# Performance work log

Hardware: AMD Instinct MI355X
Metric: run time of the kernel (lower is better)

The kernel has to match this reference:

```python
import jax, jax.numpy as jnp
import numpy as np

B, V, W, H = 512, 256, 64, 64  # batch, num_variables, window, hidden_size


def setup_inputs() -> dict:
    key = jax.random.key(0)
    ks = jax.random.split(key, 10)
    s = 0.05
    return {
        "x": jax.random.normal(ks[0], (B, V, W), dtype=jnp.float32),
        # nn.LSTM(input=V, hidden=H): gate order i, f, g, o
        "w_ih": jax.random.normal(ks[1], (4 * H, V), dtype=jnp.float32) * s,
        "w_hh": jax.random.normal(ks[2], (4 * H, H), dtype=jnp.float32) * s,
        "b_ih": jax.random.normal(ks[3], (4 * H,), dtype=jnp.float32) * s,
        "b_hh": jax.random.normal(ks[4], (4 * H,), dtype=jnp.float32) * s,
        # linear_v: Linear(window, 1, bias=False)
        "w_v": jax.random.normal(ks[5], (1, W), dtype=jnp.float32) * s,
        # linear_w: Linear(2H, window)
        "w_w": jax.random.normal(ks[6], (W, 2 * H), dtype=jnp.float32) * s,
        "b_w": jax.random.normal(ks[7], (W,), dtype=jnp.float32) * s,
        # linear_u: Linear(window, window)
        "w_u": jax.random.normal(ks[8], (W, W), dtype=jnp.float32) * s,
        "b_u": jax.random.normal(ks[9], (W,), dtype=jnp.float32) * s,
    }


def reference(x, w_ih, w_hh, b_ih, b_hh, w_v, w_w, b_w, w_u, b_u):
    batch, n_var, window = x.shape
    hidden = w_hh.shape[1]
    # linear_u over the window (last) dim: (B, V, W)
    u_out = jnp.einsum("bvw,uw->bvu", x, w_u) + b_u
    x_steps = jnp.transpose(x, (2, 0, 1))  # (W, B, V)

    def step(carry, x_t):
        h, c = carry  # each (B, H)
        # input attention
        wout = jnp.concatenate([h, c], axis=1) @ w_w.T + b_w          # (B, W)
        score = jnp.einsum("bvw,w->bv", jnp.tanh(wout[:, None, :] + u_out), w_v[0])
        alpha = jax.nn.softmax(score, axis=1)                          # (B, V)
        x_tilde = alpha * x_t                                          # (B, V)
        # LSTM cell (torch gate order i, f, g, o)
        gates = x_tilde @ w_ih.T + b_ih + h @ w_hh.T + b_hh            # (B, 4H)
        i_g, f_g, g_g, o_g = jnp.split(gates, 4, axis=1)
        i_g = jax.nn.sigmoid(i_g)
        f_g = jax.nn.sigmoid(f_g)
        g_g = jnp.tanh(g_g)
        o_g = jax.nn.sigmoid(o_g)
        c_new = f_g * c + i_g * g_g
        h_new = o_g * jnp.tanh(c_new)
        return (h_new, c_new), (x_tilde, h_new)

    init = (jnp.zeros((batch, hidden), x.dtype), jnp.zeros((batch, hidden), x.dtype))
    _, (x_tilde_seq, h_seq) = jax.lax.scan(step, init, x_steps)
    # matches torch.stack(x_tilde_list) (W,B,V) and torch.stack(h_list) (W,B,H)
    return x_tilde_seq, h_seq
```

## Files before the change

### kernel.cpp

```cpp
#include <hip/hip_runtime.h>


#define KLOG2E  1.4426950408889634f
#define K2LOG2E 2.8853900817779268f

typedef _Float16 h2 __attribute__((ext_vector_type(2)));
union H2U { h2 h; unsigned u; };

__device__ __forceinline__ float frcp(float x)  { return __builtin_amdgcn_rcpf(x); }
__device__ __forceinline__ float fexp2(float x) { return __builtin_amdgcn_exp2f(x); }
__device__ __forceinline__ float fsigmoid(float x) { return frcp(1.f + fexp2(-KLOG2E * x)); }
__device__ __forceinline__ float ftanh(float x) { return 1.f - 2.f * frcp(fexp2(K2LOG2E * x) + 1.f); }

#if __has_builtin(__builtin_amdgcn_fdot2)
__device__ __forceinline__ float fdot2(h2 a, h2 b, float c) { return __builtin_amdgcn_fdot2(a, b, c, false); }
#else
__device__ __forceinline__ float fdot2(h2 a, h2 b, float c) { return c + (float)a.x*(float)b.x + (float)a.y*(float)b.y; }
#endif

__device__ __forceinline__ unsigned pkrtz_u(float a, float b) {
#if __has_builtin(__builtin_amdgcn_cvt_pkrtz)
    H2U r; r.h = __builtin_bit_cast(h2, __builtin_amdgcn_cvt_pkrtz(a, b)); return r.u;
#else
    H2U r; r.h.x = (_Float16)a; r.h.y = (_Float16)b; return r.u;
#endif
}
__device__ __forceinline__ h2 pk_rtn(float a, float b) {
    h2 r; r.x = (_Float16)a; r.y = (_Float16)b; return r;
}

#define L_EA   0
#define L_EB   17408
#define L_PSA  34816
#define L_PSB  35328
#define L_EXFA 35840
#define L_EXFB 36096
#define L_XHA  36352
#define L_XHB  36480
#define L_EWA  36608
#define L_EWB  36672
#define L_HCA  36736
#define L_HCB  36864
#define L_HHA  36992
#define L_HHB  37024
#define L_BI   37056
#define L_WV   37312
#define L_WS   37376
#define L_TOT  37392

__global__ __launch_bounds__(512, 2) void enc_kernel(
    const float* __restrict__ x,
    const float* __restrict__ w_ih,
    const float* __restrict__ w_hh,
    const float* __restrict__ b_ih,
    const float* __restrict__ b_hh,
    const float* __restrict__ w_v,
    const float* __restrict__ w_w,
    const float* __restrict__ b_w,
    const float* __restrict__ w_u,
    const float* __restrict__ b_u,
    float* __restrict__ out_xt,
    float* __restrict__ out_h)
{
    extern __shared__ float lds[];
    float*    EA   = lds + L_EA;    float*    EB   = lds + L_EB;
    float*    psA  = lds + L_PSA;   float*    psB  = lds + L_PSB;
    float*    exfA = lds + L_EXFA;  float*    exfB = lds + L_EXFB;
    unsigned* xhA  = (unsigned*)(lds + L_XHA);
    unsigned* xhB  = (unsigned*)(lds + L_XHB);
    float*    ewA  = lds + L_EWA;   float*    ewB  = lds + L_EWB;
    float*    hcA  = lds + L_HCA;   float*    hcB  = lds + L_HCB;
    unsigned* hhA  = (unsigned*)(lds + L_HHA);
    unsigned* hhB  = (unsigned*)(lds + L_HHB);
    float*    biasL= lds + L_BI;
    float*    wv2L = lds + L_WV;
    float*    wsum = lds + L_WS;

    const int tid  = threadIdx.x;
    const int lane = tid & 63;
    const int wvi  = tid >> 6;
    const int bA   = blockIdx.x;
    const int bB   = blockIdx.x + 256;
    const int j    = tid & 255;
    const int sg   = tid >> 8;

    if (tid < 256) biasL[tid] = b_ih[tid] + b_hh[tid];
    if (tid < 64)  wv2L[tid] = -2.f * w_v[tid];
    if (tid < 128) { hcA[tid] = 0.f; hcB[tid] = 0.f; }
    if (tid < 32)  { hhA[tid] = 0u; hhB[tid] = 0u; }

    float Sv = 0.f;
#pragma unroll
    for (int wi = 0; wi < 64; ++wi) Sv += w_v[wi];
    const float bu_lane = b_u[lane];

#pragma unroll 1
    for (int bb = 0; bb < 2; ++bb) {
        float* E = bb ? EB : EA;
        const int b = bb ? bB : bA;
#pragma unroll 1
        for (int half = 0; half < 2; ++half) {
            float4 wu_r[8];
#pragma unroll
            for (int i = 0; i < 8; ++i)
                wu_r[i] = *(const float4*)&w_u[lane*64 + half*32 + 4*i];
            const float* xb = x + b*16384 + half*32;
#pragma unroll 2
            for (int vi = 0; vi < 32; ++vi) {
                int v = __builtin_amdgcn_readfirstlane(wvi*32 + vi);
                const float4* xr = (const float4*)(xb + v*64);
                float acc = 0.f;
#pragma unroll
                for (int i = 0; i < 8; ++i) {
                    float4 xx = xr[i]; float4 wu = wu_r[i];
                    acc += xx.x*wu.x + xx.y*wu.y + xx.z*wu.z + xx.w*wu.w;
                }
                if (half == 0) E[v*68 + lane] = acc + bu_lane;
                else           E[v*68 + lane] = fexp2(K2LOG2E * (E[v*68 + lane] + acc));
            }
        }
    }
    __syncthreads();

    h2 wihr2[64];
    {
        const float4* g4 = (const float4*)(w_ih + j*256 + sg*128);
#pragma unroll
        for (int i = 0; i < 32; ++i) {
            float4 v4 = g4[i];
            wihr2[2*i]     = pk_rtn(v4.x, v4.y);
            wihr2[2*i + 1] = pk_rtn(v4.z, v4.w);
        }
    }
    h2 whh2[16];
    {
        const float4* h4 = (const float4*)(w_hh + j*64 + sg*32);
#pragma unroll
        for (int i = 0; i < 8; ++i) {
            float4 v4 = h4[i];
            whh2[2*i]     = pk_rtn(v4.x, v4.y);
            whh2[2*i + 1] = pk_rtn(v4.z, v4.w);
        }
    }
    const int w8 = wvi*8 + (lane & 7);
    const int kg = lane >> 3;
    float4 www4[4];
#pragma unroll
    for (int m = 0; m < 4; ++m)
        www4[m] = *(const float4*)&w_w[w8*128 + kg*4 + 32*m];
    const float bwr = b_w[w8];

    const float* xrow = x + (sg ? bB : bA)*16384 + j*64;
    const float* Erow = (sg ? EB : EA) + j*68;
    const float* ewX  = sg ? ewB : ewA;
    float*       exfX = sg ? exfB : exfA;
    unsigned*    xhX  = sg ? xhB : xhA;
    float xcur = xrow[0];

    for (int t = 0; t < 64; ++t) {
        {
            float accA = 0.f, accB = 0.f;
#pragma unroll
            for (int m = 0; m < 4; ++m) {
                float4 w4 = www4[m];
                float4 hA = *(const float4*)&hcA[kg*4 + 32*m];
                float4 hB = *(const float4*)&hcB[kg*4 + 32*m];
                accA += hA.x*w4.x + hA.y*w4.y + hA.z*w4.z + hA.w*w4.w;
                accB += hB.x*w4.x + hB.y*w4.y + hB.z*w4.z + hB.w*w4.w;
            }
#pragma unroll
            for (int off = 8; off <= 32; off <<= 1) {
                accA += __shfl_xor(accA, off, 64);
                accB += __shfl_xor(accB, off, 64);
            }
            if (kg == 0)      ewA[w8] = fexp2(K2LOG2E * (accA + bwr));
            else if (kg == 1) ewB[w8] = fexp2(K2LOG2E * (accB + bwr));
        }
        float xnxt = (t < 63) ? xrow[t + 1] : 0.f;
        __syncthreads();

        {
            float acc = Sv;
#pragma unroll
            for (int q = 0; q < 16; ++q) {
                float4 e4 = *(const float4*)&Erow[4*q];
                float4 c4 = *(const float4*)&ewX[4*q];
                float4 v4 = *(const float4*)&wv2L[4*q];
                acc += v4.x * frcp(e4.x*c4.x + 1.f);
                acc += v4.y * frcp(e4.y*c4.y + 1.f);
                acc += v4.z * frcp(e4.z*c4.z + 1.f);
                acc += v4.w * frcp(e4.w*c4.w + 1.f);
            }
            float e  = fexp2(KLOG2E * acc);
            float ex = e * xcur;
            float s = e;
#pragma unroll
            for (int off = 1; off <= 32; off <<= 1) s += __shfl_xor(s, off, 64);
            if (lane == 0) wsum[wvi] = s;
            exfX[j] = ex;
            float exp2v = __shfl_xor(ex, 1, 64);
            if (!(lane & 1)) xhX[j >> 1] = pkrtz_u(ex, exp2v);
        }
        xcur = xnxt;
        __syncthreads();

        {
            float rA = frcp((wsum[0] + wsum[1]) + (wsum[2] + wsum[3]));
            float rB = frcp((wsum[4] + wsum[5]) + (wsum[6] + wsum[7]));
            if (sg == 0) out_xt[t*131072 + bA*256 + j] = rA * exfA[j];
            else         out_xt[t*131072 + bB*256 + j] = rB * exfB[j];

            float aA = 0.f, aB = 0.f;
            const uint4* xxA = (const uint4*)xhA + sg*16;
            const uint4* xxB = (const uint4*)xhB + sg*16;
#pragma unroll
            for (int i = 0; i < 16; ++i) {
                uint4 ua = xxA[i], ub = xxB[i];
                H2U a0, a1, a2, a3, b0, b1, b2, b3;
                a0.u = ua.x; a1.u = ua.y; a2.u = ua.z; a3.u = ua.w;
                b0.u = ub.x; b1.u = ub.y; b2.u = ub.z; b3.u = ub.w;
                aA = fdot2(a0.h, wihr2[4*i + 0], aA);
                aA = fdot2(a1.h, wihr2[4*i + 1], aA);
                aA = fdot2(a2.h, wihr2[4*i + 2], aA);
                aA = fdot2(a3.h, wihr2[4*i + 3], aA);
                aB = fdot2(b0.h, wihr2[4*i + 0], aB);
                aB = fdot2(b1.h, wihr2[4*i + 1], aB);
                aB = fdot2(b2.h, wihr2[4*i + 2], aB);
                aB = fdot2(b3.h, wihr2[4*i + 3], aB);
            }
            float ahA = 0.f, ahB = 0.f;
            const uint4* hha = (const uint4*)hhA + sg*4;
            const uint4* hhb = (const uint4*)hhB + sg*4;
#pragma unroll
            for (int i = 0; i < 4; ++i) {
                uint4 ua = hha[i], ub = hhb[i];
                H2U a0, a1, a2, a3, b0, b1, b2, b3;
                a0.u = ua.x; a1.u = ua.y; a2.u = ua.z; a3.u = ua.w;
                b0.u = ub.x; b1.u = ub.y; b2.u = ub.z; b3.u = ub.w;
                ahA = fdot2(a0.h, whh2[4*i + 0], ahA);
                ahA = fdot2(a1.h, whh2[4*i + 1], ahA);
                ahA = fdot2(a2.h, whh2[4*i + 2], ahA);
                ahA = fdot2(a3.h, whh2[4*i + 3], ahA);
                ahB = fdot2(b0.h, whh2[4*i + 0], ahB);
                ahB = fdot2(b1.h, whh2[4*i + 1], ahB);
                ahB = fdot2(b2.h, whh2[4*i + 2], ahB);
                ahB = fdot2(b3.h, whh2[4*i + 3], ahB);
            }
            psA[sg*256 + j] = rA*aA + ahA;
            psB[sg*256 + j] = rB*aB + ahB;
        }
        __syncthreads();

        if (wvi < 2) {
            float*    ps = wvi ? psB : psA;
            float*    hc = wvi ? hcB : hcA;
            unsigned* hh = wvi ? hhB : hhA;
            float*    oh = out_h + t*32768 + (wvi ? bB : bA)*64;
            const int k = lane;
            float gi = biasL[k      ] + ps[k      ] + ps[256 + k      ];
            float gf = biasL[64  + k] + ps[64  + k] + ps[256 + 64  + k];
            float gg = biasL[128 + k] + ps[128 + k] + ps[256 + 128 + k];
            float go = biasL[192 + k] + ps[192 + k] + ps[256 + 192 + k];
            gi = fsigmoid(gi); gf = fsigmoid(gf);
            gg = ftanh(gg);    go = fsigmoid(go);
            float cn = gf * hc[64 + k] + gi * gg;
            float hn = go * ftanh(cn);
            hc[k] = hn; hc[64 + k] = cn;
            float hp = __shfl_xor(hn, 1, 64);
            if (!(lane & 1)) hh[k >> 1] = pkrtz_u(hn, hp);
            oh[k] = hn;
        }
        __syncthreads();
    }
}

extern "C" void kernel_launch(void* const* d_in, const int* in_sizes, int n_in,
                              void* d_out, int out_size, void* d_ws, size_t ws_size,
                              hipStream_t stream) {
    const float* x    = (const float*)d_in[0];
    const float* w_ih = (const float*)d_in[1];
    const float* w_hh = (const float*)d_in[2];
    const float* b_ih = (const float*)d_in[3];
    const float* b_hh = (const float*)d_in[4];
    const float* w_v  = (const float*)d_in[5];
    const float* w_w  = (const float*)d_in[6];
    const float* b_w  = (const float*)d_in[7];
    const float* w_u  = (const float*)d_in[8];
    const float* b_u  = (const float*)d_in[9];

    float* out_xt = (float*)d_out;
    float* out_h  = out_xt + 64*512*256;

    const size_t shbytes = (size_t)L_TOT * sizeof(float);
    (void)hipFuncSetAttribute((const void*)enc_kernel,
                        hipFuncAttributeMaxDynamicSharedMemorySize, (int)shbytes);
    enc_kernel<<<dim3(256), dim3(512), shbytes, stream>>>(
        x, w_ih, w_hh, b_ih, b_hh, w_v, w_w, b_w, w_u, b_u, out_xt, out_h);
}
```

Before: 337.3 us.

## Double threads per block and split recurrent step work across 1024 threads

Raises the block from 512 to 1024 threads and spreads every phase of the serial recurrence over them. The attention score is split across two half-waves, the w_w projection uses 8-lane groups per output, and the gate dot products are split four ways with a larger partial-sum buffer. The aim is a shorter per-timestep critical path in the latency-bound 64-step loop. In exchange it adds more shuffles and more barrier participants, and the register budget per thread is tighter under launch_bounds(1024,1).

```diff
diff --git a/kernel.cpp b/kernel.cpp
--- a/kernel.cpp
+++ b/kernel.cpp
@@ -32,23 +32,23 @@
 #define L_EA   0
 #define L_EB   17408
 #define L_PSA  34816
-#define L_PSB  35328
-#define L_EXFA 35840
-#define L_EXFB 36096
-#define L_XHA  36352
-#define L_XHB  36480
-#define L_EWA  36608
-#define L_EWB  36672
-#define L_HCA  36736
-#define L_HCB  36864
-#define L_HHA  36992
-#define L_HHB  37024
-#define L_BI   37056
-#define L_WV   37312
-#define L_WS   37376
-#define L_TOT  37392
-
-__global__ __launch_bounds__(512, 2) void enc_kernel(
+#define L_PSB  35840
+#define L_EXFA 36864
+#define L_EXFB 37120
+#define L_XHA  37376
+#define L_XHB  37504
+#define L_EWA  37632
+#define L_EWB  37696
+#define L_HCA  37760
+#define L_HCB  37888
+#define L_HHA  38016
+#define L_HHB  38048
+#define L_BI   38080
+#define L_WV   38336
+#define L_WS   38400
+#define L_TOT  38416
+
+__global__ __launch_bounds__(1024, 1) void enc_kernel(
     const float* __restrict__ x,
     const float* __restrict__ w_ih,
     const float* __restrict__ w_hh,
@@ -81,8 +81,15 @@
     const int wvi  = tid >> 6;
     const int bA   = blockIdx.x;
     const int bB   = blockIdx.x + 256;
-    const int j    = tid & 255;
-    const int sg   = tid >> 8;
+
+    const int j4  = tid & 255;
+    const int sgq = tid >> 8;
+    const int p1b = tid >> 9;
+    const int w8  = (tid >> 3) & 63;
+    const int kg  = tid & 7;
+    const int p2b   = wvi >> 3;
+    const int v2    = ((wvi & 7) << 5) + (lane & 31);
+    const int half2 = lane >> 5;
 
     if (tid < 256) biasL[tid] = b_ih[tid] + b_hh[tid];
     if (tid < 64)  wv2L[tid] = -2.f * w_v[tid];
@@ -106,8 +113,8 @@
                 wu_r[i] = *(const float4*)&w_u[lane*64 + half*32 + 4*i];
             const float* xb = x + b*16384 + half*32;
 #pragma unroll 2
-            for (int vi = 0; vi < 32; ++vi) {
-                int v = __builtin_amdgcn_readfirstlane(wvi*32 + vi);
+            for (int vi = 0; vi < 16; ++vi) {
+                int v = __builtin_amdgcn_readfirstlane(wvi*16 + vi);
                 const float4* xr = (const float4*)(xb + v*64);
                 float acc = 0.f;
 #pragma unroll
@@ -122,99 +129,105 @@
     }
     __syncthreads();
 
-    h2 wihr2[64];
+    h2 wihr2[32];
     {
-        const float4* g4 = (const float4*)(w_ih + j*256 + sg*128);
-#pragma unroll
-        for (int i = 0; i < 32; ++i) {
+        const float4* g4 = (const float4*)(w_ih + j4*256 + sgq*64);
+#pragma unroll
+        for (int i = 0; i < 16; ++i) {
             float4 v4 = g4[i];
             wihr2[2*i]     = pk_rtn(v4.x, v4.y);
             wihr2[2*i + 1] = pk_rtn(v4.z, v4.w);
         }
     }
-    h2 whh2[16];
+    h2 whh2[8];
     {
-        const float4* h4 = (const float4*)(w_hh + j*64 + sg*32);
-#pragma unroll
-        for (int i = 0; i < 8; ++i) {
+        const float4* h4 = (const float4*)(w_hh + j4*64 + sgq*16);
+#pragma unroll
+        for (int i = 0; i < 4; ++i) {
             float4 v4 = h4[i];
             whh2[2*i]     = pk_rtn(v4.x, v4.y);
             whh2[2*i + 1] = pk_rtn(v4.z, v4.w);
         }
     }
-    const int w8 = wvi*8 + (lane & 7);
-    const int kg = lane >> 3;
-    float4 www4[4];
-#pragma unroll
-    for (int m = 0; m < 4; ++m)
-        www4[m] = *(const float4*)&w_w[w8*128 + kg*4 + 32*m];
+    float4 www0 = *(const float4*)&w_w[w8*128 + kg*8];
+    float4 www1 = *(const float4*)&w_w[w8*128 + kg*8 + 4];
     const float bwr = b_w[w8];
 
-    const float* xrow = x + (sg ? bB : bA)*16384 + j*64;
-    const float* Erow = (sg ? EB : EA) + j*68;
-    const float* ewX  = sg ? ewB : ewA;
-    float*       exfX = sg ? exfB : exfA;
-    unsigned*    xhX  = sg ? xhB : xhA;
-    float xcur = xrow[0];
+    const float* xrow = x + (p2b ? bB : bA)*16384 + v2*64;
+    float xcur = (half2 == 0) ? xrow[0] : 0.f;
 
     for (int t = 0; t < 64; ++t) {
         {
-            float accA = 0.f, accB = 0.f;
-#pragma unroll
-            for (int m = 0; m < 4; ++m) {
-                float4 w4 = www4[m];
-                float4 hA = *(const float4*)&hcA[kg*4 + 32*m];
-                float4 hB = *(const float4*)&hcB[kg*4 + 32*m];
-                accA += hA.x*w4.x + hA.y*w4.y + hA.z*w4.z + hA.w*w4.w;
-                accB += hB.x*w4.x + hB.y*w4.y + hB.z*w4.z + hB.w*w4.w;
-            }
-#pragma unroll
-            for (int off = 8; off <= 32; off <<= 1) {
-                accA += __shfl_xor(accA, off, 64);
-                accB += __shfl_xor(accB, off, 64);
-            }
-            if (kg == 0)      ewA[w8] = fexp2(K2LOG2E * (accA + bwr));
-            else if (kg == 1) ewB[w8] = fexp2(K2LOG2E * (accB + bwr));
-        }
-        float xnxt = (t < 63) ? xrow[t + 1] : 0.f;
+            const float* hcx = p1b ? hcB : hcA;
+            float4 h0 = *(const float4*)&hcx[kg*8];
+            float4 h1 = *(const float4*)&hcx[kg*8 + 4];
+            float acc = h0.x*www0.x + h0.y*www0.y + h0.z*www0.z + h0.w*www0.w
+                      + h1.x*www1.x + h1.y*www1.y + h1.z*www1.z + h1.w*www1.w;
+            acc += __shfl_xor(acc, 1, 64);
+            acc += __shfl_xor(acc, 2, 64);
+            acc += __shfl_xor(acc, 4, 64);
+            if (kg == 0) (p1b ? ewB : ewA)[w8] = fexp2(K2LOG2E * (acc + bwr));
+        }
+        float xnxt = (half2 == 0 && t < 63) ? xrow[t + 1] : 0.f;
         __syncthreads();
 
         {
-            float acc = Sv;
-#pragma unroll
-            for (int q = 0; q < 16; ++q) {
+            const float* Erow = (p2b ? EB : EA) + v2*68 + half2*32;
+            const float* ewX  = (p2b ? ewB : ewA) + half2*32;
+            const float* wvX  = wv2L + half2*32;
+            float a0 = 0.f, a1 = 0.f;
+#pragma unroll
+            for (int q = 0; q < 4; ++q) {
                 float4 e4 = *(const float4*)&Erow[4*q];
                 float4 c4 = *(const float4*)&ewX[4*q];
-                float4 v4 = *(const float4*)&wv2L[4*q];
-                acc += v4.x * frcp(e4.x*c4.x + 1.f);
-                acc += v4.y * frcp(e4.y*c4.y + 1.f);
-                acc += v4.z * frcp(e4.z*c4.z + 1.f);
-                acc += v4.w * frcp(e4.w*c4.w + 1.f);
-            }
+                float4 v4 = *(const float4*)&wvX[4*q];
+                a0 += v4.x * frcp(e4.x*c4.x + 1.f);
+                a0 += v4.y * frcp(e4.y*c4.y + 1.f);
+                a0 += v4.z * frcp(e4.z*c4.z + 1.f);
+                a0 += v4.w * frcp(e4.w*c4.w + 1.f);
+            }
+#pragma unroll
+            for (int q = 4; q < 8; ++q) {
+                float4 e4 = *(const float4*)&Erow[4*q];
+                float4 c4 = *(const float4*)&ewX[4*q];
+                float4 v4 = *(const float4*)&wvX[4*q];
+                a1 += v4.x * frcp(e4.x*c4.x + 1.f);
+                a1 += v4.y * frcp(e4.y*c4.y + 1.f);
+                a1 += v4.z * frcp(e4.z*c4.z + 1.f);
+                a1 += v4.w * frcp(e4.w*c4.w + 1.f);
+            }
+            float acc = a0 + a1 + (half2 ? 0.f : Sv);
+            acc += __shfl_xor(acc, 32, 64);
             float e  = fexp2(KLOG2E * acc);
             float ex = e * xcur;
             float s = e;
-#pragma unroll
-            for (int off = 1; off <= 32; off <<= 1) s += __shfl_xor(s, off, 64);
+            s += __shfl_xor(s, 1, 64);  s += __shfl_xor(s, 2, 64);
+            s += __shfl_xor(s, 4, 64);  s += __shfl_xor(s, 8, 64);
+            s += __shfl_xor(s, 16, 64);
             if (lane == 0) wsum[wvi] = s;
-            exfX[j] = ex;
-            float exp2v = __shfl_xor(ex, 1, 64);
-            if (!(lane & 1)) xhX[j >> 1] = pkrtz_u(ex, exp2v);
+            if (half2 == 0) {
+                (p2b ? exfB : exfA)[v2] = ex;
+                float ex2 = __shfl_xor(ex, 1, 64);
+                if (!(lane & 1)) (p2b ? xhB : xhA)[v2 >> 1] = pkrtz_u(ex, ex2);
+            }
         }
         xcur = xnxt;
         __syncthreads();
 
         {
-            float rA = frcp((wsum[0] + wsum[1]) + (wsum[2] + wsum[3]));
-            float rB = frcp((wsum[4] + wsum[5]) + (wsum[6] + wsum[7]));
-            if (sg == 0) out_xt[t*131072 + bA*256 + j] = rA * exfA[j];
-            else         out_xt[t*131072 + bB*256 + j] = rB * exfB[j];
+            float rA = ((wsum[0] + wsum[1]) + (wsum[2] + wsum[3]))
+                     + ((wsum[4] + wsum[5]) + (wsum[6] + wsum[7]));
+            float rB = ((wsum[8] + wsum[9]) + (wsum[10] + wsum[11]))
+                     + ((wsum[12] + wsum[13]) + (wsum[14] + wsum[15]));
+            rA = frcp(rA); rB = frcp(rB);
+            if (sgq == 0)      out_xt[t*131072 + bA*256 + j4] = rA * exfA[j4];
+            else if (sgq == 1) out_xt[t*131072 + bB*256 + j4] = rB * exfB[j4];
 
             float aA = 0.f, aB = 0.f;
-            const uint4* xxA = (const uint4*)xhA + sg*16;
-            const uint4* xxB = (const uint4*)xhB + sg*16;
-#pragma unroll
-            for (int i = 0; i < 16; ++i) {
+            const uint4* xxA = (const uint4*)xhA + sgq*8;
+            const uint4* xxB = (const uint4*)xhB + sgq*8;
+#pragma unroll
+            for (int i = 0; i < 8; ++i) {
                 uint4 ua = xxA[i], ub = xxB[i];
                 H2U a0, a1, a2, a3, b0, b1, b2, b3;
                 a0.u = ua.x; a1.u = ua.y; a2.u = ua.z; a3.u = ua.w;
@@ -229,10 +242,10 @@
                 aB = fdot2(b3.h, wihr2[4*i + 3], aB);
             }
             float ahA = 0.f, ahB = 0.f;
-            const uint4* hha = (const uint4*)hhA + sg*4;
-            const uint4* hhb = (const uint4*)hhB + sg*4;
-#pragma unroll
-            for (int i = 0; i < 4; ++i) {
+            const uint4* hha = (const uint4*)hhA + sgq*2;
+            const uint4* hhb = (const uint4*)hhB + sgq*2;
+#pragma unroll
+            for (int i = 0; i < 2; ++i) {
                 uint4 ua = hha[i], ub = hhb[i];
                 H2U a0, a1, a2, a3, b0, b1, b2, b3;
                 a0.u = ua.x; a1.u = ua.y; a2.u = ua.z; a3.u = ua.w;
@@ -246,8 +259,8 @@
                 ahB = fdot2(b2.h, whh2[4*i + 2], ahB);
                 ahB = fdot2(b3.h, whh2[4*i + 3], ahB);
             }
-            psA[sg*256 + j] = rA*aA + ahA;
-            psB[sg*256 + j] = rB*aB + ahB;
+            psA[sgq*256 + j4] = rA*aA + ahA;
+            psB[sgq*256 + j4] = rB*aB + ahB;
         }
         __syncthreads();
 
@@ -257,10 +270,10 @@
             unsigned* hh = wvi ? hhB : hhA;
             float*    oh = out_h + t*32768 + (wvi ? bB : bA)*64;
             const int k = lane;
-            float gi = biasL[k      ] + ps[k      ] + ps[256 + k      ];
-            float gf = biasL[64  + k] + ps[64  + k] + ps[256 + 64  + k];
-            float gg = biasL[128 + k] + ps[128 + k] + ps[256 + 128 + k];
-            float go = biasL[192 + k] + ps[192 + k] + ps[256 + 192 + k];
+            float gi = biasL[k      ] + (ps[k      ] + ps[256 + k      ]) + (ps[512 + k      ] + ps[768 + k      ]);
+            float gf = biasL[64  + k] + (ps[64  + k] + ps[320 + k      ]) + (ps[576 + k      ] + ps[832 + k      ]);
+            float gg = biasL[128 + k] + (ps[128 + k] + ps[384 + k      ]) + (ps[640 + k      ] + ps[896 + k      ]);
+            float go = biasL[192 + k] + (ps[192 + k] + ps[448 + k      ]) + (ps[704 + k      ] + ps[960 + k      ]);
             gi = fsigmoid(gi); gf = fsigmoid(gf);
             gg = ftanh(gg);    go = fsigmoid(go);
             float cn = gf * hc[64 + k] + gi * gg;
@@ -294,6 +307,6 @@
     const size_t shbytes = (size_t)L_TOT * sizeof(float);
     (void)hipFuncSetAttribute((const void*)enc_kernel,
                         hipFuncAttributeMaxDynamicSharedMemorySize, (int)shbytes);
-    enc_kernel<<<dim3(256), dim3(512), shbytes, stream>>>(
+    enc_kernel<<<dim3(256), dim3(1024), shbytes, stream>>>(
         x, w_ih, w_hh, b_ih, b_hh, w_v, w_w, b_w, w_u, b_u, out_xt, out_h);
 }
```

Measured after the change: 480.7 us. 42.5% more time.

## Use MFMA for LSTM gate GEMV and centralize softmax normalization

Applied to the files above, without the earlier changes.

Replaces the per-thread fp16 dot2 gate products with MFMA 16x16x32 f16 instructions, padding the 2-row (two batch) A-matrix to 16 rows, with weight fragments held in registers. Softmax normalization moves into a separate phase where two waves sum the exponentials and write normalized x_tilde and packed fp16 copies, in place of per-wave partial sums. This removes the heavy fdot2 register footprint and the duplicated work across the two thread groups. In exchange it adds an extra barrier per timestep and leaves most MFMA rows as wasted padding.

```diff
diff --git a/kernel.cpp b/kernel.cpp
--- a/kernel.cpp
+++ b/kernel.cpp
@@ -4,7 +4,9 @@
 #define KLOG2E  1.4426950408889634f
 #define K2LOG2E 2.8853900817779268f
 
-typedef _Float16 h2 __attribute__((ext_vector_type(2)));
+typedef _Float16 h2    __attribute__((ext_vector_type(2)));
+typedef __fp16   f16x8 __attribute__((ext_vector_type(8)));
+typedef float    f32x4 __attribute__((ext_vector_type(4)));
 union H2U { h2 h; unsigned u; };
 
 __device__ __forceinline__ float frcp(float x)  { return __builtin_amdgcn_rcpf(x); }
@@ -12,29 +14,16 @@
 __device__ __forceinline__ float fsigmoid(float x) { return frcp(1.f + fexp2(-KLOG2E * x)); }
 __device__ __forceinline__ float ftanh(float x) { return 1.f - 2.f * frcp(fexp2(K2LOG2E * x) + 1.f); }
 
-#if __has_builtin(__builtin_amdgcn_fdot2)
-__device__ __forceinline__ float fdot2(h2 a, h2 b, float c) { return __builtin_amdgcn_fdot2(a, b, c, false); }
-#else
-__device__ __forceinline__ float fdot2(h2 a, h2 b, float c) { return c + (float)a.x*(float)b.x + (float)a.y*(float)b.y; }
-#endif
-
 __device__ __forceinline__ unsigned pkrtz_u(float a, float b) {
-#if __has_builtin(__builtin_amdgcn_cvt_pkrtz)
     H2U r; r.h = __builtin_bit_cast(h2, __builtin_amdgcn_cvt_pkrtz(a, b)); return r.u;
-#else
-    H2U r; r.h.x = (_Float16)a; r.h.y = (_Float16)b; return r.u;
-#endif
-}
-__device__ __forceinline__ h2 pk_rtn(float a, float b) {
-    h2 r; r.x = (_Float16)a; r.y = (_Float16)b; return r;
 }
 
 #define L_EA   0
 #define L_EB   17408
 #define L_PSA  34816
 #define L_PSB  35328
-#define L_EXFA 35840
-#define L_EXFB 36096
+#define L_XTA  35840
+#define L_XTB  36096
 #define L_XHA  36352
 #define L_XHB  36480
 #define L_EWA  36608
@@ -45,8 +34,7 @@
 #define L_HHB  37024
 #define L_BI   37056
 #define L_WV   37312
-#define L_WS   37376
-#define L_TOT  37392
+#define L_TOT  37376
 
 __global__ __launch_bounds__(512, 2) void enc_kernel(
     const float* __restrict__ x,
@@ -65,7 +53,7 @@
     extern __shared__ float lds[];
     float*    EA   = lds + L_EA;    float*    EB   = lds + L_EB;
     float*    psA  = lds + L_PSA;   float*    psB  = lds + L_PSB;
-    float*    exfA = lds + L_EXFA;  float*    exfB = lds + L_EXFB;
+    float*    xtA  = lds + L_XTA;   float*    xtB  = lds + L_XTB;
     unsigned* xhA  = (unsigned*)(lds + L_XHA);
     unsigned* xhB  = (unsigned*)(lds + L_XHB);
     float*    ewA  = lds + L_EWA;   float*    ewB  = lds + L_EWB;
@@ -74,25 +62,53 @@
     unsigned* hhB  = (unsigned*)(lds + L_HHB);
     float*    biasL= lds + L_BI;
     float*    wv2L = lds + L_WV;
-    float*    wsum = lds + L_WS;
 
     const int tid  = threadIdx.x;
     const int lane = tid & 63;
     const int wvi  = tid >> 6;
     const int bA   = blockIdx.x;
     const int bB   = blockIdx.x + 256;
-    const int j    = tid & 255;
-    const int sg   = tid >> 8;
+
+    f16x8 wbx0[8], wbx1[8], wbh0[2], wbh1[2];
+    {
+        const int col0 = wvi*32 + (lane & 15);
+        const int col1 = col0 + 16;
+        const int kofs = (lane >> 4) * 8;
+#pragma unroll
+        for (int kk = 0; kk < 8; ++kk) {
+            const float* s0 = w_ih + col0*256 + kk*32 + kofs;
+            const float* s1 = w_ih + col1*256 + kk*32 + kofs;
+            f16x8 a, b;
+#pragma unroll
+            for (int i = 0; i < 8; ++i) { a[i] = (__fp16)s0[i]; b[i] = (__fp16)s1[i]; }
+            wbx0[kk] = a; wbx1[kk] = b;
+        }
+#pragma unroll
+        for (int kk = 0; kk < 2; ++kk) {
+            const float* s0 = w_hh + col0*64 + kk*32 + kofs;
+            const float* s1 = w_hh + col1*64 + kk*32 + kofs;
+            f16x8 a, b;
+#pragma unroll
+            for (int i = 0; i < 8; ++i) { a[i] = (__fp16)s0[i]; b[i] = (__fp16)s1[i]; }
+            wbh0[kk] = a; wbh1[kk] = b;
+        }
+    }
+    const int w8 = wvi*8 + (lane & 7);
+    const int kg = lane >> 3;
+    float4 www4[4];
+#pragma unroll
+    for (int m = 0; m < 4; ++m)
+        www4[m] = *(const float4*)&w_w[w8*128 + kg*4 + 32*m];
+    const float bwr = b_w[w8];
+    float Sv = 0.f;
+#pragma unroll
+    for (int wi = 0; wi < 64; ++wi) Sv += w_v[wi];
+    const float bu_lane = b_u[lane];
 
     if (tid < 256) biasL[tid] = b_ih[tid] + b_hh[tid];
-    if (tid < 64)  wv2L[tid] = -2.f * w_v[tid];
+    if (tid < 64) wv2L[tid] = -2.f * w_v[tid];
     if (tid < 128) { hcA[tid] = 0.f; hcB[tid] = 0.f; }
     if (tid < 32)  { hhA[tid] = 0u; hhB[tid] = 0u; }
-
-    float Sv = 0.f;
-#pragma unroll
-    for (int wi = 0; wi < 64; ++wi) Sv += w_v[wi];
-    const float bu_lane = b_u[lane];
 
 #pragma unroll 1
     for (int bb = 0; bb < 2; ++bb) {
@@ -122,39 +138,12 @@
     }
     __syncthreads();
 
-    h2 wihr2[64];
-    {
-        const float4* g4 = (const float4*)(w_ih + j*256 + sg*128);
-#pragma unroll
-        for (int i = 0; i < 32; ++i) {
-            float4 v4 = g4[i];
-            wihr2[2*i]     = pk_rtn(v4.x, v4.y);
-            wihr2[2*i + 1] = pk_rtn(v4.z, v4.w);
-        }
-    }
-    h2 whh2[16];
-    {
-        const float4* h4 = (const float4*)(w_hh + j*64 + sg*32);
-#pragma unroll
-        for (int i = 0; i < 8; ++i) {
-            float4 v4 = h4[i];
-            whh2[2*i]     = pk_rtn(v4.x, v4.y);
-            whh2[2*i + 1] = pk_rtn(v4.z, v4.w);
-        }
-    }
-    const int w8 = wvi*8 + (lane & 7);
-    const int kg = lane >> 3;
-    float4 www4[4];
-#pragma unroll
-    for (int m = 0; m < 4; ++m)
-        www4[m] = *(const float4*)&w_w[w8*128 + kg*4 + 32*m];
-    const float bwr = b_w[w8];
-
-    const float* xrow = x + (sg ? bB : bA)*16384 + j*64;
-    const float* Erow = (sg ? EB : EA) + j*68;
-    const float* ewX  = sg ? ewB : ewA;
-    float*       exfX = sg ? exfB : exfA;
-    unsigned*    xhX  = sg ? xhB : xhA;
+    const int  xj   = tid & 255;
+    const int  bsel = tid >> 8;
+    const float* xrow = x + (bsel ? bB : bA)*16384 + xj*64;
+    const float* Erow = (bsel ? EB : EA) + xj*68;
+    const float* ewX  = bsel ? ewB : ewA;
+    float*       psX  = bsel ? psB : psA;
     float xcur = xrow[0];
 
     for (int t = 0; t < 64; ++t) {
@@ -180,74 +169,76 @@
         __syncthreads();
 
         {
-            float acc = Sv;
+            float ac0 = 0.f, ac1 = 0.f, ac2 = 0.f, ac3 = 0.f;
 #pragma unroll
             for (int q = 0; q < 16; ++q) {
                 float4 e4 = *(const float4*)&Erow[4*q];
                 float4 c4 = *(const float4*)&ewX[4*q];
                 float4 v4 = *(const float4*)&wv2L[4*q];
-                acc += v4.x * frcp(e4.x*c4.x + 1.f);
-                acc += v4.y * frcp(e4.y*c4.y + 1.f);
-                acc += v4.z * frcp(e4.z*c4.z + 1.f);
-                acc += v4.w * frcp(e4.w*c4.w + 1.f);
-            }
+                ac0 += v4.x * frcp(e4.x*c4.x + 1.f);
+                ac1 += v4.y * frcp(e4.y*c4.y + 1.f);
+                ac2 += v4.z * frcp(e4.z*c4.z + 1.f);
+                ac3 += v4.w * frcp(e4.w*c4.w + 1.f);
+            }
+            float acc = Sv + ((ac0 + ac1) + (ac2 + ac3));
             float e  = fexp2(KLOG2E * acc);
-            float ex = e * xcur;
-            float s = e;
-#pragma unroll
-            for (int off = 1; off <= 32; off <<= 1) s += __shfl_xor(s, off, 64);
-            if (lane == 0) wsum[wvi] = s;
-            exfX[j] = ex;
-            float exp2v = __shfl_xor(ex, 1, 64);
-            if (!(lane & 1)) xhX[j >> 1] = pkrtz_u(ex, exp2v);
+            psX[xj]       = e;
+            psX[256 + xj] = e * xcur;
         }
         xcur = xnxt;
         __syncthreads();
 
+        if (wvi < 2) {
+            float*    ps = wvi ? psB : psA;
+            float*    xt = wvi ? xtB : xtA;
+            unsigned* xh = wvi ? xhB : xhA;
+            float4 ev = *(const float4*)&ps[4*lane];
+            float4 ex = *(const float4*)&ps[256 + 4*lane];
+            float sum = (ev.x + ev.y) + (ev.z + ev.w);
+#pragma unroll
+            for (int off = 1; off <= 32; off <<= 1) sum += __shfl_xor(sum, off, 64);
+            float r = frcp(sum);
+            float4 xo;
+            xo.x = ex.x*r; xo.y = ex.y*r; xo.z = ex.z*r; xo.w = ex.w*r;
+            *(float4*)&xt[4*lane] = xo;
+            xh[2*lane]     = pkrtz_u(xo.x, xo.y);
+            xh[2*lane + 1] = pkrtz_u(xo.z, xo.w);
+        }
+        __syncthreads();
+
         {
-            float rA = frcp((wsum[0] + wsum[1]) + (wsum[2] + wsum[3]));
-            float rB = frcp((wsum[4] + wsum[5]) + (wsum[6] + wsum[7]));
-            if (sg == 0) out_xt[t*131072 + bA*256 + j] = rA * exfA[j];
-            else         out_xt[t*131072 + bB*256 + j] = rB * exfB[j];
-
-            float aA = 0.f, aB = 0.f;
-            const uint4* xxA = (const uint4*)xhA + sg*16;
-            const uint4* xxB = (const uint4*)xhB + sg*16;
-#pragma unroll
-            for (int i = 0; i < 16; ++i) {
-                uint4 ua = xxA[i], ub = xxB[i];
-                H2U a0, a1, a2, a3, b0, b1, b2, b3;
-                a0.u = ua.x; a1.u = ua.y; a2.u = ua.z; a3.u = ua.w;
-                b0.u = ub.x; b1.u = ub.y; b2.u = ub.z; b3.u = ub.w;
-                aA = fdot2(a0.h, wihr2[4*i + 0], aA);
-                aA = fdot2(a1.h, wihr2[4*i + 1], aA);
-                aA = fdot2(a2.h, wihr2[4*i + 2], aA);
-                aA = fdot2(a3.h, wihr2[4*i + 3], aA);
-                aB = fdot2(b0.h, wihr2[4*i + 0], aB);
-                aB = fdot2(b1.h, wihr2[4*i + 1], aB);
-                aB = fdot2(b2.h, wihr2[4*i + 2], aB);
-                aB = fdot2(b3.h, wihr2[4*i + 3], aB);
-            }
-            float ahA = 0.f, ahB = 0.f;
-            const uint4* hha = (const uint4*)hhA + sg*4;
-            const uint4* hhb = (const uint4*)hhB + sg*4;
-#pragma unroll
-            for (int i = 0; i < 4; ++i) {
-                uint4 ua = hha[i], ub = hhb[i];
-                H2U a0, a1, a2, a3, b0, b1, b2, b3;
-                a0.u = ua.x; a1.u = ua.y; a2.u = ua.z; a3.u = ua.w;
-                b0.u = ub.x; b1.u = ub.y; b2.u = ub.z; b3.u = ub.w;
-                ahA = fdot2(a0.h, whh2[4*i + 0], ahA);
-                ahA = fdot2(a1.h, whh2[4*i + 1], ahA);
-                ahA = fdot2(a2.h, whh2[4*i + 2], ahA);
-                ahA = fdot2(a3.h, whh2[4*i + 3], ahA);
-                ahB = fdot2(b0.h, whh2[4*i + 0], ahB);
-                ahB = fdot2(b1.h, whh2[4*i + 1], ahB);
-                ahB = fdot2(b2.h, whh2[4*i + 2], ahB);
-                ahB = fdot2(b3.h, whh2[4*i + 3], ahB);
-            }
-            psA[sg*256 + j] = rA*aA + ahA;
-            psB[sg*256 + j] = rB*aB + ahB;
+            float xtv = bsel ? xtB[xj] : xtA[xj];
+            out_xt[t*131072 + (bsel ? bB : bA)*256 + xj] = xtv;
+
+            const int row = lane & 15;
+            const int q4  = (lane >> 4) * 4;
+            f32x4 ax0 = {0.f,0.f,0.f,0.f}, ax1 = {0.f,0.f,0.f,0.f};
+            f32x4 ah0 = {0.f,0.f,0.f,0.f}, ah1 = {0.f,0.f,0.f,0.f};
+            const unsigned* xsrc = (row == 1) ? xhB : xhA;
+#pragma unroll
+            for (int kk = 0; kk < 8; ++kk) {
+                f16x8 a = {};
+                if (row < 2)
+                    a = __builtin_bit_cast(f16x8, *(const uint4*)(xsrc + kk*16 + q4));
+                ax0 = __builtin_amdgcn_mfma_f32_16x16x32_f16(a, wbx0[kk], ax0, 0, 0, 0);
+                ax1 = __builtin_amdgcn_mfma_f32_16x16x32_f16(a, wbx1[kk], ax1, 0, 0, 0);
+            }
+            const unsigned* hsrc = (row == 1) ? hhB : hhA;
+#pragma unroll
+            for (int kk = 0; kk < 2; ++kk) {
+                f16x8 a = {};
+                if (row < 2)
+                    a = __builtin_bit_cast(f16x8, *(const uint4*)(hsrc + kk*16 + q4));
+                ah0 = __builtin_amdgcn_mfma_f32_16x16x32_f16(a, wbh0[kk], ah0, 0, 0, 0);
+                ah1 = __builtin_amdgcn_mfma_f32_16x16x32_f16(a, wbh1[kk], ah1, 0, 0, 0);
+            }
+            if (lane < 16) {
+                const int j0 = wvi*32 + lane, j1 = j0 + 16;
+                psA[j0] = ax0[0] + ah0[0];
+                psA[j1] = ax1[0] + ah1[0];
+                psB[j0] = ax0[1] + ah0[1];
+                psB[j1] = ax1[1] + ah1[1];
+            }
         }
         __syncthreads();
 
@@ -257,12 +248,10 @@
             unsigned* hh = wvi ? hhB : hhA;
             float*    oh = out_h + t*32768 + (wvi ? bB : bA)*64;
             const int k = lane;
-            float gi = biasL[k      ] + ps[k      ] + ps[256 + k      ];
-            float gf = biasL[64  + k] + ps[64  + k] + ps[256 + 64  + k];
-            float gg = biasL[128 + k] + ps[128 + k] + ps[256 + 128 + k];
-            float go = biasL[192 + k] + ps[192 + k] + ps[256 + 192 + k];
-            gi = fsigmoid(gi); gf = fsigmoid(gf);
-            gg = ftanh(gg);    go = fsigmoid(go);
+            float gi = fsigmoid(biasL[k      ] + ps[k      ]);
+            float gf = fsigmoid(biasL[64  + k] + ps[64  + k]);
+            float gg = ftanh   (biasL[128 + k] + ps[128 + k]);
+            float go = fsigmoid(biasL[192 + k] + ps[192 + k]);
             float cn = gf * hc[64 + k] + gi * gg;
             float hn = go * ftanh(cn);
             hc[k] = hn; hc[64 + k] = cn;
```

Result: faster. 281.6 us (-16.5%).
